# Kernel tuning notes

Measured on AMD Instinct MI355X. Metric: run time of the kernel, lower is better.

The kernel has to match this reference:

```python
import jax, jax.numpy as jnp
import numpy as np

D_MODEL = 1024
NUM_HEADS = 16
THETA = 10000.0
BATCH = 2
SEQ = 2048


def setup_inputs() -> dict:
    key = jax.random.key(0)
    ks = jax.random.split(key, 5)
    std = (2.0 / (D_MODEL + D_MODEL)) ** 0.5
    mk = lambda k: jax.random.truncated_normal(k, -3.0, 3.0, (D_MODEL, D_MODEL), jnp.float32) * std
    return {
        'x': jax.random.normal(ks[0], (BATCH, SEQ, D_MODEL), jnp.float32),
        'Wq': mk(ks[1]),
        'Wk': mk(ks[2]),
        'Wv': mk(ks[3]),
        'Wo': mk(ks[4]),
        'token_positions': jnp.arange(SEQ, dtype=jnp.int32),
    }


def _apply_rope(x, token_positions, theta):
    # x: (B, H, S, d_k)
    d_k = x.shape[-1]
    freq = 1.0 / theta ** (jnp.arange(0, d_k, 2, dtype=jnp.float32) / d_k)  # (d_k//2,)
    freqs = token_positions.astype(jnp.float32)[:, None] * freq[None, :]   # (S, d_k//2)
    cos, sin = jnp.cos(freqs), jnp.sin(freqs)
    x_real = x[..., 0::2]
    x_imag = x[..., 1::2]
    rot_real = x_real * cos - x_imag * sin
    rot_imag = x_real * sin + x_imag * cos
    # interleave back: (..., d_k//2, 2) -> (..., d_k)
    out = jnp.stack([rot_real, rot_imag], axis=-1)
    return out.reshape(x.shape)


def reference(x, Wq, Wk, Wv, Wo, token_positions):
    B, S, D = x.shape
    H = NUM_HEADS
    d_k = D // H

    def split_heads(t):
        return t.reshape(B, S, H, d_k).transpose(0, 2, 1, 3)  # (B, H, S, d_k)

    Q = split_heads(jnp.einsum('bsd,od->bso', x, Wq))
    K = split_heads(jnp.einsum('bsd,od->bso', x, Wk))
    V = split_heads(jnp.einsum('bsd,od->bso', x, Wv))

    Q = _apply_rope(Q, token_positions, THETA)
    K = _apply_rope(K, token_positions, THETA)

    # naive materialized attention with causal mask, faithful to source
    scores = jnp.einsum('bhqd,bhkd->bhqk', Q, K)
    causal = jnp.tril(jnp.ones((S, S), dtype=bool))  # True = attend
    scores = jnp.where(causal[None, None], scores, -jnp.inf)
    scores = scores / jnp.sqrt(jnp.asarray(d_k, scores.dtype))
    probs = jax.nn.softmax(scores, axis=-1)
    attn = jnp.einsum('bhqk,bhkd->bhqd', probs, V)  # (B, H, S, d_v)

    attn = attn.transpose(0, 2, 1, 3).reshape(B, S, D)
    return jnp.einsum('bsd,od->bso', attn, Wo)
```

## Files before the change

### kernel.cpp

```cpp
#include <hip/hip_runtime.h>
#include <hip/hip_bf16.h>
#include <math.h>

#define NUM_HEADS 16
#define DK 64
#define SEQ 2048
#define BATCHN 2
#define DM 1024
#define BS (BATCHN*SEQ)
#define LSCALE 0.18033688011112042f

typedef __bf16 bf16x8 __attribute__((ext_vector_type(8)));
typedef float floatx4 __attribute__((ext_vector_type(4)));
typedef unsigned short ushort;
typedef unsigned int uint;

__device__ __forceinline__ ushort f2bu(float f){
    union { __hip_bfloat16 h; ushort u; } cv; cv.h = __float2bfloat16(f); return cv.u;
}
__device__ __forceinline__ uint packbf(float a, float b){
    return (uint)f2bu(a) | ((uint)f2bu(b) << 16);
}
__device__ __forceinline__ float bu2f(ushort u){
    union { uint u; float f; } cv; cv.u = (uint)u << 16; return cv.f;
}
__device__ __forceinline__ uint cvtpk(float lo, float hi){
    uint r; asm("v_cvt_pk_bf16_f32 %0, %1, %2" : "=v"(r) : "v"(lo), "v"(hi));
    return r;
}
__device__ __forceinline__ void gl16(const void* g, void* l){
    __builtin_amdgcn_global_load_lds(
        (const __attribute__((address_space(1))) unsigned int*)g,
        (__attribute__((address_space(3))) unsigned int*)l, 16, 0, 0);
}

__global__ __launch_bounds__(256)
void castall(const float* __restrict__ x,  const float* __restrict__ wq,
             const float* __restrict__ wk, const float* __restrict__ wv,
             const float* __restrict__ wo, const int* __restrict__ pos,
             ushort* __restrict__ xb, ushort* __restrict__ wqkb,
             ushort* __restrict__ wvb, ushort* __restrict__ wob,
             float2* __restrict__ tab)
{
    int bid = blockIdx.x;
    if (bid >= 4096) {
        int idx = (bid - 4096)*256 + threadIdx.x;
        int s = idx >> 5, i = idx & 31;
        float invf = expf(-0.28782313662425575f * (float)i);
        float ang = (float)pos[s] * invf;
        float sn, cs; sincosf(ang, &sn, &cs);
        tab[idx] = make_float2(cs, sn);
        return;
    }
    const float* src; ushort* dst; int off;
    if (bid < 2048)      { src = x;  dst = xb;             off = bid; }
    else if (bid < 2560) { src = wq; dst = wqkb;           off = bid - 2048; }
    else if (bid < 3072) { src = wk; dst = wqkb + 1048576; off = bid - 2560; }
    else if (bid < 3584) { src = wv; dst = wvb;            off = bid - 3072; }
    else                 { src = wo; dst = wob;            off = bid - 3584; }
    int i = off*2048 + threadIdx.x*8;
    float4 a = *(const float4*)(src+i);
    float4 b = *(const float4*)(src+i+4);
    uint4 o;
    o.x = packbf(a.x, a.y);
    o.y = packbf(a.z, a.w);
    o.z = packbf(b.x, b.y);
    o.w = packbf(b.z, b.w);
    *(uint4*)(dst+i) = o;
}

__global__ __launch_bounds__(256)
void proj_fused(const ushort* __restrict__ xb, const ushort* __restrict__ Wqkb,
                const ushort* __restrict__ Wvb, ushort* __restrict__ Qb,
                ushort* __restrict__ VTp, const float2* __restrict__ rope)
{
    __shared__ ushort As[128*64];
    __shared__ ushort Bs[128*64];

    const int bx = blockIdx.x;
    int bid;
    if (bx < 512) {
        const int xcd = bx & 7, i = bx >> 3;
        const int tr = (xcd >> 1)*8 + (i >> 3);
        const int tc = (xcd & 1)*8 + (i & 7);
        bid = tr*16 + tc;
    } else {
        const int j = bx - 512;
        const int xcd = j & 7, i = j >> 3;
        const int tr = i >> 2;
        const int tc = xcd*4 + (i & 3);
        bid = 512 + tr*32 + tc;
    }

    const ushort* A; const ushort* W; int row0, col0, mode;
    if (bid < 512) { A = xb;  W = Wqkb; row0 = (bid >> 4) * 128;
                     col0 = (bid & 15) * 128;  mode = 1; }
    else           { int i = bid - 512; A = Wvb; W = xb;
                     row0 = (i >> 5) * 128; col0 = (i & 31) * 128; mode = 2; }

    const int t = threadIdx.x;
    const int w = t >> 6;
    const int L = t & 63;
    const int lr = L & 15;
    const int lq = L >> 4;
    const int wrow = w * 32;

    floatx4 acc[2][8];
    #pragma unroll
    for (int i = 0; i < 2; ++i)
        #pragma unroll
        for (int j = 0; j < 8; ++j)
            acc[i][j] = (floatx4){0.f,0.f,0.f,0.f};

    const int rr = t >> 3;
    const int ko = ((t & 7) ^ (rr & 7)) * 8;
    const ushort* ga = A + (size_t)(row0 + rr) * DM + ko;
    const ushort* gb = W + (size_t)(col0 + rr) * DM + ko;
    ushort* Asl = As + t*8;
    ushort* Bsl = Bs + t*8;

    for (int k0 = 0; k0 < DM; k0 += 64) {
        __syncthreads();
        gl16(ga + k0,                 Asl);
        gl16(ga + k0 + (size_t)32*DM, Asl + 2048);
        gl16(ga + k0 + (size_t)64*DM, Asl + 4096);
        gl16(ga + k0 + (size_t)96*DM, Asl + 6144);
        gl16(gb + k0,                 Bsl);
        gl16(gb + k0 + (size_t)32*DM, Bsl + 2048);
        gl16(gb + k0 + (size_t)64*DM, Bsl + 4096);
        gl16(gb + k0 + (size_t)96*DM, Bsl + 6144);
        __syncthreads();

        #pragma unroll
        for (int h = 0; h < 2; ++h) {
            const int co = (lq*8 + h*32) ^ ((lr & 7) << 3);
            bf16x8 aF0 = *(const bf16x8*)&As[(wrow + lr)*64 + co];
            bf16x8 aF1 = *(const bf16x8*)&As[(wrow + 16 + lr)*64 + co];
            #pragma unroll
            for (int tc = 0; tc < 8; ++tc) {
                bf16x8 bF = *(const bf16x8*)&Bs[(tc*16 + lr)*64 + co];
                acc[0][tc] = __builtin_amdgcn_mfma_f32_16x16x32_bf16(aF0, bF, acc[0][tc], 0, 0, 0);
                acc[1][tc] = __builtin_amdgcn_mfma_f32_16x16x32_bf16(aF1, bF, acc[1][tc], 0, 0, 0);
            }
        }
    }

    if (mode == 2) {
        #pragma unroll
        for (int tr = 0; tr < 2; ++tr)
            #pragma unroll
            for (int tc = 0; tc < 8; ++tc)
                #pragma unroll
                for (int r = 0; r < 4; ++r) {
                    int m = row0 + wrow + tr*16 + lq*4 + r;
                    int c = col0 + tc*16 + lr;
                    VTp[(size_t)m * BS + c] = f2bu(acc[tr][tc][r]);
                }
    } else {
        const int mat = col0 >> 10;
        const int base_hh = (col0 & 1023) >> 6;
        ushort* out = Qb + (size_t)mat * (BATCHN*NUM_HEADS*SEQ*DK);
        const float qscale = mat ? 1.f : LSCALE;
        #pragma unroll
        for (int tr = 0; tr < 2; ++tr)
            #pragma unroll
            for (int tc = 0; tc < 8; ++tc)
                #pragma unroll
                for (int r = 0; r < 4; ++r) {
                    int m = row0 + wrow + tr*16 + lq*4 + r;
                    int b = m >> 11;
                    int s = m & (SEQ - 1);
                    int dd = (tc*16 + lr) & 63;
                    int hh = base_hh + (tc >> 2);
                    float v = acc[tr][tc][r];
                    float o = __shfl_xor(v, 1, 64);
                    float2 cs = rope[s*32 + (dd >> 1)];
                    float rv = (dd & 1) ? fmaf(o, cs.y,  v * cs.x)
                                        : fmaf(-o, cs.y, v * cs.x);
                    out[((size_t)((b*NUM_HEADS + hh)*SEQ + s))*DK + dd] =
                        f2bu(rv * qscale);
                }
    }
}

__global__ __launch_bounds__(256)
void gemm_out(const ushort* __restrict__ A, const ushort* __restrict__ W,
              float* __restrict__ out)
{
    __shared__ ushort As[128*64];
    __shared__ ushort Bs[64*64];

    const int t = threadIdx.x;
    const int w = t >> 6;
    const int L = t & 63;
    const int lr = L & 15;
    const int lq = L >> 4;
    const int row0 = blockIdx.y * 128;
    const int col0 = blockIdx.x * 64;
    const int wrow = w * 32;

    floatx4 acc[2][4];
    #pragma unroll
    for (int i = 0; i < 2; ++i)
        #pragma unroll
        for (int j = 0; j < 4; ++j)
            acc[i][j] = (floatx4){0.f,0.f,0.f,0.f};

    const int rr = t >> 3;
    const int ko = ((t & 7) ^ (rr & 7)) * 8;
    const ushort* ga = A + (size_t)(row0 + rr) * DM + ko;
    const ushort* gb = W + (size_t)(col0 + rr) * DM + ko;
    ushort* Asl = As + t*8;
    ushort* Bsl = Bs + t*8;

    for (int k0 = 0; k0 < DM; k0 += 64) {
        __syncthreads();
        gl16(ga + k0,                 Asl);
        gl16(ga + k0 + (size_t)32*DM, Asl + 2048);
        gl16(ga + k0 + (size_t)64*DM, Asl + 4096);
        gl16(ga + k0 + (size_t)96*DM, Asl + 6144);
        gl16(gb + k0,                 Bsl);
        gl16(gb + k0 + (size_t)32*DM, Bsl + 2048);
        __syncthreads();

        #pragma unroll
        for (int h = 0; h < 2; ++h) {
            const int co = (lq*8 + h*32) ^ ((lr & 7) << 3);
            bf16x8 aF0 = *(const bf16x8*)&As[(wrow + lr)*64 + co];
            bf16x8 aF1 = *(const bf16x8*)&As[(wrow + 16 + lr)*64 + co];
            #pragma unroll
            for (int tc = 0; tc < 4; ++tc) {
                bf16x8 bF = *(const bf16x8*)&Bs[(tc*16 + lr)*64 + co];
                acc[0][tc] = __builtin_amdgcn_mfma_f32_16x16x32_bf16(aF0, bF, acc[0][tc], 0, 0, 0);
                acc[1][tc] = __builtin_amdgcn_mfma_f32_16x16x32_bf16(aF1, bF, acc[1][tc], 0, 0, 0);
            }
        }
    }

    #pragma unroll
    for (int tr = 0; tr < 2; ++tr)
        #pragma unroll
        for (int tc = 0; tc < 4; ++tc)
            #pragma unroll
            for (int r = 0; r < 4; ++r) {
                int m = row0 + wrow + tr*16 + lq*4 + r;
                int c = col0 + tc*16 + lr;
                out[(size_t)m * DM + c] = acc[tr][tc][r];
            }
}

__global__ __launch_bounds__(128)
void attn_mfma(const ushort* __restrict__ Qb, const ushort* __restrict__ Kb,
               const ushort* __restrict__ VT, ushort* __restrict__ attnb,
               ushort* __restrict__ Opart, float* __restrict__ lpart)
{
    __shared__ ushort Ks[64*64];
    __shared__ ushort Vs[64*64];

    const int t = threadIdx.x;
    const int w = t >> 6;
    const int L = t & 63;
    const int lr = L & 15, lq = L >> 4;
    const int h  = blockIdx.y;
    const int b  = blockIdx.z;

    int qt, chunk, nch;
    {
        const int bx = blockIdx.x;
        if (bx < 8)       { qt = bx;              chunk = 0;     nch = 1; }
        else if (bx < 24) { int i = bx - 8;  qt = 8  + (i>>1); chunk = i&1;        nch = 2; }
        else if (bx < 48) { int i = bx - 24; int q3 = i/3; qt = 16 + q3; chunk = i - q3*3; nch = 3; }
        else              { int i = bx - 48; qt = 24 + (i>>2); chunk = i&3;        nch = 4; }
    }
    const int nt = qt + 1;
    const int t0 = (nt * chunk) / nch;
    const int t1 = (nt * (chunk + 1)) / nch;
    const int q0 = qt * 64;
    const int qw = q0 + w * 32;
    const size_t qkbase = (size_t)(b*NUM_HEADS + h) * SEQ * DK;

    bf16x8 qA0, qA1, qB0, qB1;
    {
        const ushort* qp = Qb + qkbase + (size_t)(qw + lr) * DK + lq*8;
        qA0 = *(const bf16x8*)qp;
        qA1 = *(const bf16x8*)(qp + 32);
        qB0 = *(const bf16x8*)(qp + 16*DK);
        qB1 = *(const bf16x8*)(qp + 16*DK + 32);
    }

    bf16x8 ones8;
    {
        union { uint u[4]; bf16x8 v; } o;
        o.u[0] = o.u[1] = o.u[2] = o.u[3] = 0x3f803f80u;
        ones8 = o.v;
    }

    floatx4 O0[4], O1[4];
    #pragma unroll
    for (int g = 0; g < 4; ++g) {
        O0[g] = (floatx4){0.f,0.f,0.f,0.f};
        O1[g] = (floatx4){0.f,0.f,0.f,0.f};
    }
    floatx4 lA = (floatx4){0.f,0.f,0.f,0.f};
    floatx4 lB = (floatx4){0.f,0.f,0.f,0.f};

    const int sr = t >> 3, t7 = t & 7;
    const int kwb  = (sr*64 + t7*8) ^ ((sr & 7) << 3);
    const int pc0  = ((t7 >> 2) << 3) | ((t7 & 1) << 2) | ((t7 >> 1) & 1);
    const int vwb0 = (sr*64 + pc0*4)     ^ ((sr & 7) << 3);
    const int vwb1 = (sr*64 + pc0*4 + 8) ^ ((sr & 7) << 3);
    const ushort* kpt = Kb + qkbase + (size_t)sr * DK + t7*8;
    const ushort* vpt = VT + ((size_t)(h*DK + sr)) * BS + b*SEQ + t7*8;

    const int kro0 = (lr*64 + lq*8)      ^ ((lr & 7) << 3);
    const int kro1 = (lr*64 + 32 + lq*8) ^ ((lr & 7) << 3);

    uint4 kv0, kv1, kv2, kv3, vv0, vv1, vv2, vv3;

#define GLOAD(T)                                                              \
    {                                                                         \
        const ushort* kg = kpt + (size_t)(T) * 64 * DK;                       \
        const ushort* vg = vpt + (T) * 64;                                    \
        kv0 = *(const uint4*)(kg);                                            \
        kv1 = *(const uint4*)(kg + 16*DK);                                    \
        kv2 = *(const uint4*)(kg + 32*DK);                                    \
        kv3 = *(const uint4*)(kg + 48*DK);                                    \
        vv0 = *(const uint4*)(vg);                                            \
        vv1 = *(const uint4*)(vg + (size_t)16*BS);                            \
        vv2 = *(const uint4*)(vg + (size_t)32*BS);                            \
        vv3 = *(const uint4*)(vg + (size_t)48*BS);                            \
    }

#define STAGE()                                                               \
    {                                                                         \
        *(uint4*)&Ks[kwb]        = kv0;                                       \
        *(uint4*)&Ks[kwb + 1024] = kv1;                                       \
        *(uint4*)&Ks[kwb + 2048] = kv2;                                       \
        *(uint4*)&Ks[kwb + 3072] = kv3;                                       \
        *(uint2*)&Vs[vwb0]        = make_uint2(vv0.x, vv0.y);                 \
        *(uint2*)&Vs[vwb1]        = make_uint2(vv0.z, vv0.w);                 \
        *(uint2*)&Vs[vwb0 + 1024] = make_uint2(vv1.x, vv1.y);                 \
        *(uint2*)&Vs[vwb1 + 1024] = make_uint2(vv1.z, vv1.w);                 \
        *(uint2*)&Vs[vwb0 + 2048] = make_uint2(vv2.x, vv2.y);                 \
        *(uint2*)&Vs[vwb1 + 2048] = make_uint2(vv2.z, vv2.w);                 \
        *(uint2*)&Vs[vwb0 + 3072] = make_uint2(vv3.x, vv3.y);                 \
        *(uint2*)&Vs[vwb1 + 3072] = make_uint2(vv3.z, vv3.w);                 \
    }

#define COMPUTE(LASTT)                                                        \
    {                                                                         \
        uint2 pk0[4], pk1[4];                                                 \
        _Pragma("unroll")                                                     \
        for (int g = 0; g < 4; ++g) {                                         \
            bf16x8 kf0 = *(const bf16x8*)&Ks[kro0 + g*1024];                  \
            bf16x8 kf1 = *(const bf16x8*)&Ks[kro1 + g*1024];                  \
            floatx4 s0 = (floatx4){0.f,0.f,0.f,0.f};                          \
            s0 = __builtin_amdgcn_mfma_f32_16x16x32_bf16(kf0, qA0, s0,0,0,0); \
            s0 = __builtin_amdgcn_mfma_f32_16x16x32_bf16(kf1, qA1, s0,0,0,0); \
            floatx4 s1 = (floatx4){0.f,0.f,0.f,0.f};                          \
            s1 = __builtin_amdgcn_mfma_f32_16x16x32_bf16(kf0, qB0, s1,0,0,0); \
            s1 = __builtin_amdgcn_mfma_f32_16x16x32_bf16(kf1, qB1, s1,0,0,0); \
            float a0 = __builtin_amdgcn_exp2f(s0[0]);                         \
            float a1 = __builtin_amdgcn_exp2f(s0[1]);                         \
            float a2 = __builtin_amdgcn_exp2f(s0[2]);                         \
            float a3 = __builtin_amdgcn_exp2f(s0[3]);                         \
            float b0 = __builtin_amdgcn_exp2f(s1[0]);                         \
            float b1 = __builtin_amdgcn_exp2f(s1[1]);                         \
            float b2 = __builtin_amdgcn_exp2f(s1[2]);                         \
            float b3 = __builtin_amdgcn_exp2f(s1[3]);                         \
            if (LASTT) {                                                      \
                const int kbase = g*16 + lq*4;                                \
                a0 = (kbase + 0 <= lim0) ? a0 : 0.f;                          \
                a1 = (kbase + 1 <= lim0) ? a1 : 0.f;                          \
                a2 = (kbase + 2 <= lim0) ? a2 : 0.f;                          \
                a3 = (kbase + 3 <= lim0) ? a3 : 0.f;                          \
                b0 = (kbase + 0 <= lim1) ? b0 : 0.f;                          \
                b1 = (kbase + 1 <= lim1) ? b1 : 0.f;                          \
                b2 = (kbase + 2 <= lim1) ? b2 : 0.f;                          \
                b3 = (kbase + 3 <= lim1) ? b3 : 0.f;                          \
            }                                                                 \
            pk0[g] = make_uint2(cvtpk(a0, a1), cvtpk(a2, a3));                \
            pk1[g] = make_uint2(cvtpk(b0, b1), cvtpk(b2, b3));                \
        }                                                                     \
        _Pragma("unroll")                                                     \
        for (int c = 0; c < 2; ++c) {                                         \
            union { uint u[4]; bf16x8 v; } a0u, a1u;                          \
            a0u.u[0] = pk0[2*c].x;   a0u.u[1] = pk0[2*c].y;                   \
            a0u.u[2] = pk0[2*c+1].x; a0u.u[3] = pk0[2*c+1].y;                 \
            a1u.u[0] = pk1[2*c].x;   a1u.u[1] = pk1[2*c].y;                   \
            a1u.u[2] = pk1[2*c+1].x; a1u.u[3] = pk1[2*c+1].y;                 \
            lA = __builtin_amdgcn_mfma_f32_16x16x32_bf16(a0u.v, ones8, lA,0,0,0); \
            lB = __builtin_amdgcn_mfma_f32_16x16x32_bf16(a1u.v, ones8, lB,0,0,0); \
            const int vro = c ? kro1 : kro0;                                  \
            _Pragma("unroll")                                                 \
            for (int g2 = 0; g2 < 4; ++g2) {                                  \
                bf16x8 vf = *(const bf16x8*)&Vs[vro + g2*1024];               \
                O0[g2] = __builtin_amdgcn_mfma_f32_16x16x32_bf16(a0u.v, vf, O0[g2],0,0,0); \
                O1[g2] = __builtin_amdgcn_mfma_f32_16x16x32_bf16(a1u.v, vf, O1[g2],0,0,0); \
            }                                                                 \
        }                                                                     \
    }

    GLOAD(t0);
    const bool haslast = (t1 == nt);
    const int tmain = haslast ? t1 - 1 : t1;
    {
        const int lim0 = 0, lim1 = 0;
        for (int tile = t0; tile < tmain; ++tile) {
            __syncthreads();
            STAGE();
            __syncthreads();
            if (tile + 1 < t1) GLOAD(tile + 1);
            COMPUTE(false);
        }
    }
    if (haslast) {
        __syncthreads();
        STAGE();
        __syncthreads();
        const int lim0 = qw + lr - (nt - 1)*64;
        const int lim1 = lim0 + 16;
        COMPUTE(true);
    }
#undef GLOAD
#undef STAGE
#undef COMPUTE

    if (nch == 1) {
        #pragma unroll
        for (int r = 0; r < 4; ++r) {
            float li0 = 1.f / lA[r];
            float li1 = 1.f / lB[r];
            int s0r = qw + lq*4 + r;
            int s1r = qw + 16 + lq*4 + r;
            #pragma unroll
            for (int g2 = 0; g2 < 4; ++g2) {
                attnb[((size_t)(b*SEQ + s0r))*DM + h*DK + g2*16 + lr] = f2bu(O0[g2][r] * li0);
                attnb[((size_t)(b*SEQ + s1r))*DM + h*DK + g2*16 + lr] = f2bu(O1[g2][r] * li1);
            }
        }
    } else {
        const int slot = ((b*NUM_HEADS + h)*24 + (qt - 8))*4 + chunk;
        ushort* Op = Opart + (size_t)slot * 4096;
        #pragma unroll
        for (int r = 0; r < 4; ++r) {
            int ql0 = w*32 + lq*4 + r;
            int ql1 = w*32 + 16 + lq*4 + r;
            #pragma unroll
            for (int g2 = 0; g2 < 4; ++g2) {
                Op[ql0*64 + g2*16 + lr] = f2bu(O0[g2][r]);
                Op[ql1*64 + g2*16 + lr] = f2bu(O1[g2][r]);
            }
        }
        if (lr == 0) {
            #pragma unroll
            for (int r = 0; r < 4; ++r) {
                lpart[(size_t)slot*64 + w*32 + lq*4 + r]      = lA[r];
                lpart[(size_t)slot*64 + w*32 + 16 + lq*4 + r] = lB[r];
            }
        }
    }
}

__global__ __launch_bounds__(256)
void combine(const ushort* __restrict__ Opart, const float* __restrict__ lpart,
             ushort* __restrict__ attnb)
{
    int gx = blockIdx.x;
    int qti = gx % 24, bh = gx / 24;
    int h = bh & 15, b = bh >> 4;
    int qt = 8 + qti;
    int nch = (qt >> 3) + 1;
    int tid = threadIdx.x;
    int row = tid >> 2, c0 = (tid & 3) * 16;
    const int base_slot = (bh*24 + qti)*4;

    float acc[16];
    #pragma unroll
    for (int e = 0; e < 16; ++e) acc[e] = 0.f;
    float l = 0.f;

    for (int c = 0; c < nch; ++c) {
        const ushort* Op = Opart + (size_t)(base_slot + c)*4096 + row*64 + c0;
        uint4 u0 = *(const uint4*)(Op);
        uint4 u1 = *(const uint4*)(Op + 8);
        const ushort* h0 = (const ushort*)&u0;
        const ushort* h1 = (const ushort*)&u1;
        #pragma unroll
        for (int e = 0; e < 8; ++e) { acc[e]   += bu2f(h0[e]); }
        #pragma unroll
        for (int e = 0; e < 8; ++e) { acc[8+e] += bu2f(h1[e]); }
        l += lpart[(size_t)(base_slot + c)*64 + row];
    }
    float li = 1.f / l;
    int s = qt*64 + row;
    ushort* dst = attnb + ((size_t)(b*SEQ + s))*DM + h*DK + c0;
    #pragma unroll
    for (int e = 0; e < 16; ++e) dst[e] = f2bu(acc[e] * li);
}

extern "C" void kernel_launch(void* const* d_in, const int* in_sizes, int n_in,
                              void* d_out, int out_size, void* d_ws, size_t ws_size,
                              hipStream_t stream) {
    const float* x   = (const float*)d_in[0];
    const float* Wq  = (const float*)d_in[1];
    const float* Wk  = (const float*)d_in[2];
    const float* Wv  = (const float*)d_in[3];
    const float* Wo  = (const float*)d_in[4];
    const int*   pos = (const int*)d_in[5];
    float* out = (float*)d_out;

    const size_t MB = 1u << 20;
    char* ws = (char*)d_ws;
    ushort* xb    = (ushort*)(ws);
    ushort* Wqkb  = (ushort*)(ws +  8*MB);
    ushort* Wvb   = (ushort*)(ws + 12*MB);
    ushort* Opart = (ushort*)(ws);
    float*  lpart = (float*)(ws + 24*MB);
    ushort* Qb    = (ushort*)(ws + 25*MB);
    ushort* Kb    = (ushort*)(ws + 33*MB);
    ushort* VT    = (ushort*)(ws + 41*MB);
    ushort* attnb = (ushort*)(ws + 49*MB);
    float2* ropeT = (float2*)(ws + 57*MB);
    ushort* Wob   = (ushort*)(ws + 58*MB);

    dim3 blk(256);
    castall<<<4352, blk, 0, stream>>>(x, Wq, Wk, Wv, Wo, pos,
                                      xb, Wqkb, Wvb, Wob, ropeT);

    proj_fused<<<768, blk, 0, stream>>>(xb, Wqkb, Wvb, Qb, VT, ropeT);

    attn_mfma<<<dim3(80, NUM_HEADS, BATCHN), dim3(128), 0, stream>>>(Qb, Kb, VT, attnb,
                                                                     Opart, lpart);
    combine<<<768, blk, 0, stream>>>(Opart, lpart, attnb);

    gemm_out<<<dim3(16,32), blk, 0, stream>>>(attnb, Wob, out);
}
```

Baseline: 189.4 us.

## Double-buffer projection GEMM LDS tiles with K=32 stages and async prefetch

```diff
diff --git a/kernel.cpp b/kernel.cpp
--- a/kernel.cpp
+++ b/kernel.cpp
@@ -74,8 +74,8 @@
                 const ushort* __restrict__ Wvb, ushort* __restrict__ Qb,
                 ushort* __restrict__ VTp, const float2* __restrict__ rope)
 {
-    __shared__ ushort As[128*64];
-    __shared__ ushort Bs[128*64];
+    __shared__ ushort As[2*128*32];
+    __shared__ ushort Bs[2*128*32];
 
     const int bx = blockIdx.x;
     int bid;
@@ -112,38 +112,42 @@
         for (int j = 0; j < 8; ++j)
             acc[i][j] = (floatx4){0.f,0.f,0.f,0.f};
 
-    const int rr = t >> 3;
-    const int ko = ((t & 7) ^ (rr & 7)) * 8;
+    const int rr = t >> 2, ko = (t & 3) * 8;
     const ushort* ga = A + (size_t)(row0 + rr) * DM + ko;
     const ushort* gb = W + (size_t)(col0 + rr) * DM + ko;
-    ushort* Asl = As + t*8;
-    ushort* Bsl = Bs + t*8;
-
-    for (int k0 = 0; k0 < DM; k0 += 64) {
-        __syncthreads();
-        gl16(ga + k0,                 Asl);
-        gl16(ga + k0 + (size_t)32*DM, Asl + 2048);
-        gl16(ga + k0 + (size_t)64*DM, Asl + 4096);
-        gl16(ga + k0 + (size_t)96*DM, Asl + 6144);
-        gl16(gb + k0,                 Bsl);
-        gl16(gb + k0 + (size_t)32*DM, Bsl + 2048);
-        gl16(gb + k0 + (size_t)64*DM, Bsl + 4096);
-        gl16(gb + k0 + (size_t)96*DM, Bsl + 6144);
-        __syncthreads();
-
-        #pragma unroll
-        for (int h = 0; h < 2; ++h) {
-            const int co = (lq*8 + h*32) ^ ((lr & 7) << 3);
-            bf16x8 aF0 = *(const bf16x8*)&As[(wrow + lr)*64 + co];
-            bf16x8 aF1 = *(const bf16x8*)&As[(wrow + 16 + lr)*64 + co];
-            #pragma unroll
-            for (int tc = 0; tc < 8; ++tc) {
-                bf16x8 bF = *(const bf16x8*)&Bs[(tc*16 + lr)*64 + co];
-                acc[0][tc] = __builtin_amdgcn_mfma_f32_16x16x32_bf16(aF0, bF, acc[0][tc], 0, 0, 0);
-                acc[1][tc] = __builtin_amdgcn_mfma_f32_16x16x32_bf16(aF1, bF, acc[1][tc], 0, 0, 0);
-            }
+    const int ldst = rr*32 + ko;
+
+#define STG(BUF, K0)                                                          \
+    {                                                                         \
+        gl16(ga + (K0),                 &As[(BUF)*4096 + ldst]);              \
+        gl16(ga + (K0) + (size_t)64*DM, &As[(BUF)*4096 + 2048 + ldst]);       \
+        gl16(gb + (K0),                 &Bs[(BUF)*4096 + ldst]);              \
+        gl16(gb + (K0) + (size_t)64*DM, &Bs[(BUF)*4096 + 2048 + ldst]);       \
+    }
+
+    STG(0, 0)
+    asm volatile("s_waitcnt vmcnt(0)" ::: "memory");
+    __builtin_amdgcn_s_barrier();
+
+    int cur = 0;
+    for (int k0 = 0; k0 < DM; k0 += 32) {
+        if (k0 + 32 < DM) STG(cur ^ 1, k0 + 32)
+
+        const ushort* Ac = As + cur*4096;
+        const ushort* Bc = Bs + cur*4096;
+        bf16x8 aF0 = *(const bf16x8*)&Ac[(wrow + lr)*32 + lq*8];
+        bf16x8 aF1 = *(const bf16x8*)&Ac[(wrow + 16 + lr)*32 + lq*8];
+        #pragma unroll
+        for (int tc = 0; tc < 8; ++tc) {
+            bf16x8 bF = *(const bf16x8*)&Bc[(tc*16 + lr)*32 + lq*8];
+            acc[0][tc] = __builtin_amdgcn_mfma_f32_16x16x32_bf16(aF0, bF, acc[0][tc], 0, 0, 0);
+            acc[1][tc] = __builtin_amdgcn_mfma_f32_16x16x32_bf16(aF1, bF, acc[1][tc], 0, 0, 0);
         }
-    }
+        asm volatile("s_waitcnt vmcnt(0) lgkmcnt(0)" ::: "memory");
+        __builtin_amdgcn_s_barrier();
+        cur ^= 1;
+    }
+#undef STG
 
     if (mode == 2) {
         #pragma unroll
```

Result: no change. 192.2 us (+1.5%).
